# Kernel tuning notes

Measured on AMD Instinct MI355X. Metric: run time of the kernel, lower is better.

Reference implementation:

```python
import jax, jax.numpy as jnp
import numpy as np

B, C, H, W, CR = 8, 256, 128, 128, 32


def setup_inputs() -> dict:
    key = jax.random.key(0)
    ks = jax.random.split(key, 5)
    s = 0.05  # weight scale ~ conv init
    return {
        "x": jax.random.normal(ks[0], (B, C, H, W), jnp.float32),
        "Wq": jax.random.normal(ks[1], (CR, C), jnp.float32) * s,
        "bq": jnp.zeros((CR,), jnp.float32),
        "Wk": jax.random.normal(ks[2], (CR, C), jnp.float32) * s,
        "bk": jnp.zeros((CR,), jnp.float32),
        "Wv": jax.random.normal(ks[3], (CR, C), jnp.float32) * s,
        "bv": jnp.zeros((CR,), jnp.float32),
        "Wz": jax.random.normal(ks[4], (C, CR), jnp.float32) * s,
        "bz": jnp.zeros((C,), jnp.float32),
    }


def _conv1x1(w, b, x):
    # 1x1 conv == per-pixel channel matmul
    return jnp.einsum('oc,bchw->bohw', w, x) + b[None, :, None, None]


def reference(x, Wq, bq, Wk, bk, Wv, bv, Wz, bz):
    h = x.shape[2]
    q = _conv1x1(Wq, bq, x)   # (B,Cr,H,W)
    k = _conv1x1(Wk, bk, x)
    v = _conv1x1(Wv, bv, x)
    # column (height-axis) energies, -inf on diagonal to avoid double-counting self
    neg_inf_diag = jnp.where(jnp.eye(h, dtype=bool), -jnp.inf, 0.0)  # (H,H)
    energy_H = jnp.einsum('bchw,bciw->bwhi', q, k) + neg_inf_diag   # (B,W,H,H)
    energy_H = energy_H.transpose(0, 2, 1, 3)                        # (B,H,W,H)
    # row (width-axis) energies
    energy_W = jnp.einsum('bchw,bchj->bhwj', q, k)                   # (B,H,W,W)
    attn = jax.nn.softmax(jnp.concatenate([energy_H, energy_W], axis=-1), axis=-1)
    out = jnp.einsum('bciw,bhwi->bchw', v, attn[..., :h])
    out = out + jnp.einsum('bchj,bhwj->bchw', v, attn[..., h:])
    out = _conv1x1(Wz, bz, out)
    return out + x  # with_residual=True
```

## Files before the change

kernel.cpp:

```cpp
#include <hip/hip_runtime.h>
#include <stdint.h>


typedef __attribute__((ext_vector_type(8))) short bf16x8;
typedef __attribute__((ext_vector_type(4))) float f32x4;
union frag_u { uint4 u4; bf16x8 h8; };

__device__ __forceinline__ float bf2f(uint32_t u) {
  union { uint32_t i; float f; } v; v.i = u << 16; return v.f;
}
__device__ __forceinline__ float bf2f_hi(uint32_t u) {
  union { uint32_t i; float f; } v; v.i = u & 0xffff0000u; return v.f;
}
__device__ __forceinline__ uint32_t f2bf(float f) {
  union { float f; uint32_t i; } v; v.f = f;
  return (v.i + 0x7fffu + ((v.i >> 16) & 1u)) >> 16;
}
__device__ __forceinline__ void unpack8(uint4 a, float* f) {
  f[0] = bf2f(a.x); f[1] = bf2f_hi(a.x);
  f[2] = bf2f(a.y); f[3] = bf2f_hi(a.y);
  f[4] = bf2f(a.z); f[5] = bf2f_hi(a.z);
  f[6] = bf2f(a.w); f[7] = bf2f_hi(a.w);
}
__device__ __forceinline__ float ld_any(const void* p, int i, int isf32) {
  return isf32 ? ((const float*)p)[i] : bf2f(((const uint16_t*)p)[i]);
}

#define XS_SWZ(m, k)  ((m) * 40 + ((k) ^ ((((m) >> 3) & 3) << 3)))
#define P_SWZ(r, c)   ((r) * 128 + ((c) ^ (((r) & 7) << 3)))

__global__ void detect_kernel(const uint16_t* __restrict__ x, int* __restrict__ flag) {
  __shared__ int bad;
  if (threadIdx.x == 0) bad = 0;
  __syncthreads();
  int hit = 0;
#pragma unroll
  for (int s = 0; s < 16; ++s) {
    uint32_t u = x[(threadIdx.x * 16 + s) * 2];
    uint32_t e = (u >> 7) & 0xffu;
    if (e == 0u || e == 255u) hit = 1;
  }
  if (hit) atomicAdd(&bad, 1);
  __syncthreads();
  if (threadIdx.x == 0) flag[0] = (bad > 0) ? 1 : 0;
}

__global__ void prep_kernel(
    const int* __restrict__ flag,
    const void* __restrict__ Wq, const void* __restrict__ bq,
    const void* __restrict__ Wk, const void* __restrict__ bk,
    const void* __restrict__ Wv, const void* __restrict__ bv,
    const void* __restrict__ Wz, const void* __restrict__ bz,
    float* __restrict__ wb, float* __restrict__ wzf,
    float* __restrict__ bzf, uint16_t* __restrict__ wbf)
{
  int isf32 = flag[0];
  int t = blockIdx.x * 256 + threadIdx.x;
  if (t < 24576) {
    int n = t >> 8, kk = t & 255;
    int z = n >> 5, o = n & 31;
    const void* W = (z == 0) ? Wq : (z == 1) ? Wk : Wv;
    wbf[t] = (uint16_t)f2bf(ld_any(W, o * 256 + kk, isf32));
  }
  if (t < 96) {
    int z = t >> 5, o = t & 31;
    const void* bb = (z == 0) ? bq : (z == 1) ? bk : bv;
    wb[t] = ld_any(bb, o, isf32);
  }
  if (t < 8192) wzf[t] = ld_any(Wz, t, isf32);
  if (t < 256)  bzf[t] = ld_any(bz, t, isf32);
}

__global__ __launch_bounds__(256) void qkv_mfma(
    const int* __restrict__ flag, const void* __restrict__ x,
    const uint16_t* __restrict__ wbf, const float* __restrict__ wb,
    uint16_t* __restrict__ qcol, uint16_t* __restrict__ kcol,
    uint16_t* __restrict__ vcol, uint16_t* __restrict__ qrow,
    uint16_t* __restrict__ krow, uint16_t* __restrict__ vrow)
{
  __shared__ __align__(16) uint16_t Xs[128 * 40];
  int isf32 = flag[0];
  int bx = blockIdx.x;
  int b = bx >> 7, hrow = bx & 127;
  int t = threadIdx.x;
  int wv = t >> 6, L = t & 63, quad = L >> 4, l15 = L & 15;

  f32x4 acc[2][6];
#pragma unroll
  for (int mi = 0; mi < 2; ++mi)
#pragma unroll
    for (int nt = 0; nt < 6; ++nt) {
      f32x4 z0 = {0.f, 0.f, 0.f, 0.f};
      acc[mi][nt] = z0;
    }

  for (int kc = 0; kc < 8; ++kc) {
    int k0 = kc * 32;
    __syncthreads();
    if (isf32) {
      const float* xp = (const float*)x + ((size_t)b << 22)
                      + (size_t)k0 * 16384 + hrow * 128;
#pragma unroll
      for (int r = 0; r < 16; ++r) {
        int idx = r * 256 + t, k = idx >> 7, m = idx & 127;
        Xs[XS_SWZ(m, k)] = (uint16_t)f2bf(xp[(size_t)k * 16384 + m]);
      }
    } else {
      const uint16_t* xp = (const uint16_t*)x + ((size_t)b << 22)
                         + (size_t)k0 * 16384 + hrow * 128;
#pragma unroll
      for (int r = 0; r < 16; ++r) {
        int idx = r * 256 + t, k = idx >> 7, m = idx & 127;
        Xs[XS_SWZ(m, k)] = xp[(size_t)k * 16384 + m];
      }
    }
    __syncthreads();

    bf16x8 af[2];
#pragma unroll
    for (int mi = 0; mi < 2; ++mi) {
      int row = (wv * 2 + mi) * 16 + l15;
      frag_u fu;
      fu.u4 = *(const uint4*)(Xs + XS_SWZ(row, quad * 8));
      af[mi] = fu.h8;
    }
#pragma unroll
    for (int nt = 0; nt < 6; ++nt) {
      frag_u bu;
      bu.u4 = *(const uint4*)(wbf + (nt * 16 + l15) * 256 + k0 + quad * 8);
#pragma unroll
      for (int mi = 0; mi < 2; ++mi)
        acc[mi][nt] = __builtin_amdgcn_mfma_f32_16x16x32_bf16(af[mi], bu.h8, acc[mi][nt], 0, 0, 0);
    }
  }

#pragma unroll
  for (int nt = 0; nt < 6; ++nt) {
    int n = nt * 16 + l15;
    float bias = wb[n];
    int z = nt >> 1;
    int no = n & 31;
    uint16_t* colb = (z == 0) ? qcol : (z == 1) ? kcol : vcol;
    uint16_t* rowb = (z == 0) ? qrow : (z == 1) ? krow : vrow;
    size_t rowbase = (size_t)(b * 128 + hrow) * 4096;
#pragma unroll
    for (int mi = 0; mi < 2; ++mi) {
#pragma unroll
      for (int r = 0; r < 4; ++r) {
        int m = (wv * 2 + mi) * 16 + quad * 4 + r;
        uint16_t val = (uint16_t)f2bf(acc[mi][nt][r] + bias);
        rowb[rowbase + (size_t)m * 32 + no] = val;
        colb[(size_t)(b * 128 + m) * 4096 + hrow * 32 + no] = val;
      }
    }
  }
}

__global__ __launch_bounds__(256, 4) void attn_kernel(
    const uint16_t* __restrict__ q, const uint16_t* __restrict__ k,
    const uint16_t* __restrict__ v, uint16_t* __restrict__ O,
    float* __restrict__ s, int iscol)
{
  __shared__ __align__(16) uint16_t P[128 * 128];
  __shared__ __align__(16) uint16_t vT[32 * 128];

  int cid = blockIdx.x, b = cid >> 7, loc = cid & 127;
  int tid = threadIdx.x;
  const uint16_t* qc = q + (size_t)cid * 4096;
  const uint16_t* kc = k + (size_t)cid * 4096;
  const uint16_t* vc = v + (size_t)cid * 4096;

  for (int idx = tid; idx < 4096; idx += 256) {
    int ch = idx & 31, i = idx >> 5;
    vT[P_SWZ(ch, i)] = vc[idx];
  }

  int wv = tid >> 6, L = tid & 63, quad = L >> 4, l15 = L & 15;

  bf16x8 aq[2];
#pragma unroll
  for (int mi = 0; mi < 2; ++mi) {
    frag_u fu;
    fu.u4 = *(const uint4*)(qc + ((wv * 2 + mi) * 16 + l15) * 32 + quad * 8);
    aq[mi] = fu.h8;
  }
  for (int nt = 0; nt < 8; ++nt) {
    frag_u bu;
    bu.u4 = *(const uint4*)(kc + (nt * 16 + l15) * 32 + quad * 8);
    int col = nt * 16 + l15;
#pragma unroll
    for (int mi = 0; mi < 2; ++mi) {
      f32x4 z0 = {0.f, 0.f, 0.f, 0.f};
      f32x4 d = __builtin_amdgcn_mfma_f32_16x16x32_bf16(aq[mi], bu.h8, z0, 0, 0, 0);
      int row0 = (wv * 2 + mi) * 16 + quad * 4;
#pragma unroll
      for (int r = 0; r < 4; ++r) {
        float pe = __expf(d[r]);
        if (iscol && (row0 + r) == col) pe = 0.f;
        P[P_SWZ(row0 + r, col)] = (uint16_t)f2bf(pe);
      }
    }
  }
  __syncthreads();

  {
    int row = tid >> 1, hh = tid & 1;
    float ss = 0.f;
    const uint2* pr = (const uint2*)(P + row * 128 + hh * 64);
#pragma unroll 4
    for (int j = 0; j < 16; ++j) {
      uint2 u = pr[j];
      ss += bf2f(u.x); ss += bf2f_hi(u.x);
      ss += bf2f(u.y); ss += bf2f_hi(u.y);
    }
    ss += __shfl_xor(ss, 1);
    if (hh == 0) {
      size_t sbase = (size_t)b * 16384 + (iscol ? loc : loc * 128);
      s[sbase + (size_t)row * (iscol ? 128 : 1)] = ss;
    }
  }

  f32x4 acc[2][2];
#pragma unroll
  for (int mi = 0; mi < 2; ++mi)
#pragma unroll
    for (int ni = 0; ni < 2; ++ni) {
      f32x4 z0 = {0.f, 0.f, 0.f, 0.f};
      acc[mi][ni] = z0;
    }
#pragma unroll
  for (int kk = 0; kk < 4; ++kk) {
    bf16x8 ap[2], bv2[2];
#pragma unroll
    for (int mi = 0; mi < 2; ++mi) {
      int row = (wv * 2 + mi) * 16 + l15;
      frag_u fu;
      fu.u4 = *(const uint4*)(P + P_SWZ(row, kk * 32 + quad * 8));
      ap[mi] = fu.h8;
    }
#pragma unroll
    for (int ni = 0; ni < 2; ++ni) {
      int ch = ni * 16 + l15;
      frag_u fu;
      fu.u4 = *(const uint4*)(vT + P_SWZ(ch, kk * 32 + quad * 8));
      bv2[ni] = fu.h8;
    }
#pragma unroll
    for (int mi = 0; mi < 2; ++mi)
#pragma unroll
      for (int ni = 0; ni < 2; ++ni)
        acc[mi][ni] = __builtin_amdgcn_mfma_f32_16x16x32_bf16(ap[mi], bv2[ni], acc[mi][ni], 0, 0, 0);
  }

  size_t obase = (size_t)b * 524288 + (size_t)(iscol ? loc * 32 : loc * 4096);
  int orstride = iscol ? 4096 : 32;
#pragma unroll
  for (int mi = 0; mi < 2; ++mi)
#pragma unroll
    for (int ni = 0; ni < 2; ++ni) {
      int col = ni * 16 + l15;
#pragma unroll
      for (int r = 0; r < 4; ++r) {
        int row = (wv * 2 + mi) * 16 + quad * 4 + r;
        O[obase + (size_t)row * orstride + col] = (uint16_t)f2bf(acc[mi][ni][r]);
      }
    }
}

#define CSPLIT 4
__global__ __launch_bounds__(256) void combine_zres(
    const int* __restrict__ flag, const void* __restrict__ x,
    const uint16_t* __restrict__ Ocol, const uint16_t* __restrict__ Orow,
    const float* __restrict__ scol, const float* __restrict__ srow,
    const float* __restrict__ wzf, const float* __restrict__ bzf,
    void* __restrict__ out)
{
  int isf32 = flag[0];
  int bid = blockIdx.x;
  int pixblk = bid & 511;
  int cgrp = bid >> 9;
  int p = pixblk * 256 + threadIdx.x;
  int b = p >> 14;
  int rem = p & 16383;

  float inv = 1.0f / (scol[p] + srow[p]);
  float of[32];
  const uint4* c4 = (const uint4*)(Ocol + (size_t)p * 32);
  const uint4* r4 = (const uint4*)(Orow + (size_t)p * 32);
#pragma unroll
  for (int g = 0; g < 4; ++g) {
    float a[8], bb[8];
    unpack8(c4[g], a);
    unpack8(r4[g], bb);
#pragma unroll
    for (int j = 0; j < 8; ++j) of[g * 8 + j] = (a[j] + bb[j]) * inv;
  }

  int c0 = cgrp * (256 / CSPLIT);
  int c1 = c0 + (256 / CSPLIT);

  if (isf32) {
    const float* xp = (const float*)x + ((size_t)b << 22) + rem;
    float* op = (float*)out + ((size_t)b << 22) + rem;
#pragma unroll 2
    for (int c = c0; c < c1; ++c) {
      const float* wc = wzf + c * 32;
      float xv = xp[(size_t)c << 14];
      float a0 = 0.f, a1 = 0.f, a2 = 0.f, a3 = 0.f;
#pragma unroll
      for (int r = 0; r < 8; ++r) {
        a0 += wc[r]      * of[r];
        a1 += wc[8 + r]  * of[8 + r];
        a2 += wc[16 + r] * of[16 + r];
        a3 += wc[24 + r] * of[24 + r];
      }
      op[(size_t)c << 14] = bzf[c] + (a0 + a1) + (a2 + a3) + xv;
    }
  } else {
    const uint16_t* xp = (const uint16_t*)x + ((size_t)b << 22) + rem;
    uint16_t* op = (uint16_t*)out + ((size_t)b << 22) + rem;
#pragma unroll 2
    for (int c = c0; c < c1; ++c) {
      const float* wc = wzf + c * 32;
      float xv = bf2f(xp[(size_t)c << 14]);
      float a0 = 0.f, a1 = 0.f, a2 = 0.f, a3 = 0.f;
#pragma unroll
      for (int r = 0; r < 8; ++r) {
        a0 += wc[r]      * of[r];
        a1 += wc[8 + r]  * of[8 + r];
        a2 += wc[16 + r] * of[16 + r];
        a3 += wc[24 + r] * of[24 + r];
      }
      float acci = bzf[c] + (a0 + a1) + (a2 + a3) + xv;
      op[(size_t)c << 14] = (uint16_t)f2bf(acci);
    }
  }
}

extern "C" void kernel_launch(void* const* d_in, const int* in_sizes, int n_in,
                              void* d_out, int out_size, void* d_ws, size_t ws_size,
                              hipStream_t stream) {
  char* ws = (char*)d_ws;
  int*   flag = (int*)(ws);
  float* wb   = (float*)(ws + 256);
  float* wzf  = (float*)(ws + 1024);
  float* bzf  = (float*)(ws + 33792);
  uint16_t* wbf = (uint16_t*)(ws + 34816);
  uint16_t* qt = (uint16_t*)(ws + 147456);
  uint16_t* kt = qt + 4194304;
  uint16_t* vt = kt + 4194304;
  uint16_t* qr = vt + 4194304;
  uint16_t* kr = qr + 4194304;
  uint16_t* vr = kr + 4194304;
  uint16_t* Ocol = (uint16_t*)(ws + 50479104);
  uint16_t* Orow = (uint16_t*)(ws + 58867712);
  float* scol = (float*)(ws + 67256320);
  float* srow = (float*)(ws + 67780608);

  detect_kernel<<<1, 256, 0, stream>>>((const uint16_t*)d_in[0], flag);
  prep_kernel<<<96, 256, 0, stream>>>(flag, d_in[1], d_in[2], d_in[3], d_in[4],
                                      d_in[5], d_in[6], d_in[7], d_in[8],
                                      wb, wzf, bzf, wbf);
  qkv_mfma<<<1024, 256, 0, stream>>>(flag, d_in[0], wbf, wb,
                                     qt, kt, vt, qr, kr, vr);
  attn_kernel<<<1024, 256, 0, stream>>>(qt, kt, vt, Ocol, scol, 1);
  attn_kernel<<<1024, 256, 0, stream>>>(qr, kr, vr, Orow, srow, 0);
  combine_zres<<<512 * CSPLIT, 256, 0, stream>>>(flag, d_in[0], Ocol, Orow,
                                                 scol, srow, wzf, bzf, d_out);
}
```

Before: 345.1 us.

## Prefetch x tiles into registers, merge attention launches, tweak unroll and bounds

The QKV projection kernel now loads the next 32-channel chunk of x into registers while MFMAs run on the current chunk held in shared memory. This software-pipelines global loads against compute. The column and row attention passes are merged into a single 2048-block launch, with the block index choosing which pass it runs, which removes one launch and the tail between them. Separately, qkv_mfma gets a min-blocks launch bound and the combine loop unroll goes from 2 to 4. Both raise register pressure, and the 16-register prefetch buffer could cap occupancy.

Result: no change. 340.0 us (-1.5%).

```diff
diff --git a/kernel.cpp b/kernel.cpp
--- a/kernel.cpp
+++ b/kernel.cpp
@@ -71,7 +71,7 @@
   if (t < 256)  bzf[t] = ld_any(bz, t, isf32);
 }
 
-__global__ __launch_bounds__(256) void qkv_mfma(
+__global__ __launch_bounds__(256, 4) void qkv_mfma(
     const int* __restrict__ flag, const void* __restrict__ x,
     const uint16_t* __restrict__ wbf, const float* __restrict__ wb,
     uint16_t* __restrict__ qcol, uint16_t* __restrict__ kcol,
@@ -84,6 +84,10 @@
   int b = bx >> 7, hrow = bx & 127;
   int t = threadIdx.x;
   int wv = t >> 6, L = t & 63, quad = L >> 4, l15 = L & 15;
+  int m_t = t & 127, kh = t >> 7;
+
+  const float*    xf = (const float*)x    + ((size_t)b << 22) + hrow * 128 + m_t;
+  const uint16_t* xh = (const uint16_t*)x + ((size_t)b << 22) + hrow * 128 + m_t;
 
   f32x4 acc[2][6];
 #pragma unroll
@@ -94,28 +98,37 @@
       acc[mi][nt] = z0;
     }
 
+  uint32_t xs[16];
+  auto issue = [&](int kcn) {
+    if (isf32) {
+#pragma unroll
+      for (int r = 0; r < 16; ++r)
+        xs[r] = __float_as_uint(xf[(size_t)(kcn * 32 + 2 * r + kh) * 16384]);
+    } else {
+#pragma unroll
+      for (int r = 0; r < 16; ++r)
+        xs[r] = xh[(size_t)(kcn * 32 + 2 * r + kh) * 16384];
+    }
+  };
+
+  issue(0);
+
   for (int kc = 0; kc < 8; ++kc) {
-    int k0 = kc * 32;
     __syncthreads();
     if (isf32) {
-      const float* xp = (const float*)x + ((size_t)b << 22)
-                      + (size_t)k0 * 16384 + hrow * 128;
-#pragma unroll
-      for (int r = 0; r < 16; ++r) {
-        int idx = r * 256 + t, k = idx >> 7, m = idx & 127;
-        Xs[XS_SWZ(m, k)] = (uint16_t)f2bf(xp[(size_t)k * 16384 + m]);
-      }
+#pragma unroll
+      for (int r = 0; r < 16; ++r)
+        Xs[XS_SWZ(m_t, 2 * r + kh)] = (uint16_t)f2bf(__uint_as_float(xs[r]));
     } else {
-      const uint16_t* xp = (const uint16_t*)x + ((size_t)b << 22)
-                         + (size_t)k0 * 16384 + hrow * 128;
-#pragma unroll
-      for (int r = 0; r < 16; ++r) {
-        int idx = r * 256 + t, k = idx >> 7, m = idx & 127;
-        Xs[XS_SWZ(m, k)] = xp[(size_t)k * 16384 + m];
-      }
+#pragma unroll
+      for (int r = 0; r < 16; ++r)
+        Xs[XS_SWZ(m_t, 2 * r + kh)] = (uint16_t)xs[r];
     }
     __syncthreads();
 
+    if (kc < 7) issue(kc + 1);
+
+    int k0 = kc * 32;
     bf16x8 af[2];
 #pragma unroll
     for (int mi = 0; mi < 2; ++mi) {
@@ -157,18 +170,24 @@
 }
 
 __global__ __launch_bounds__(256, 4) void attn_kernel(
-    const uint16_t* __restrict__ q, const uint16_t* __restrict__ k,
-    const uint16_t* __restrict__ v, uint16_t* __restrict__ O,
-    float* __restrict__ s, int iscol)
+    const uint16_t* __restrict__ qc_, const uint16_t* __restrict__ kc_,
+    const uint16_t* __restrict__ vc_, const uint16_t* __restrict__ qr_,
+    const uint16_t* __restrict__ kr_, const uint16_t* __restrict__ vr_,
+    uint16_t* __restrict__ Ocol, uint16_t* __restrict__ Orow,
+    float* __restrict__ scol, float* __restrict__ srow)
 {
   __shared__ __align__(16) uint16_t P[128 * 128];
   __shared__ __align__(16) uint16_t vT[32 * 128];
 
-  int cid = blockIdx.x, b = cid >> 7, loc = cid & 127;
+  int bidx = blockIdx.x;
+  int iscol = (bidx < 1024) ? 1 : 0;
+  int cid = bidx & 1023, b = cid >> 7, loc = cid & 127;
   int tid = threadIdx.x;
-  const uint16_t* qc = q + (size_t)cid * 4096;
-  const uint16_t* kc = k + (size_t)cid * 4096;
-  const uint16_t* vc = v + (size_t)cid * 4096;
+  const uint16_t* qc = (iscol ? qc_ : qr_) + (size_t)cid * 4096;
+  const uint16_t* kc = (iscol ? kc_ : kr_) + (size_t)cid * 4096;
+  const uint16_t* vc = (iscol ? vc_ : vr_) + (size_t)cid * 4096;
+  uint16_t* O = iscol ? Ocol : Orow;
+  float*    s = iscol ? scol : srow;
 
   for (int idx = tid; idx < 4096; idx += 256) {
     int ch = idx & 31, i = idx >> 5;
@@ -302,7 +321,7 @@
   if (isf32) {
     const float* xp = (const float*)x + ((size_t)b << 22) + rem;
     float* op = (float*)out + ((size_t)b << 22) + rem;
-#pragma unroll 2
+#pragma unroll 4
     for (int c = c0; c < c1; ++c) {
       const float* wc = wzf + c * 32;
       float xv = xp[(size_t)c << 14];
@@ -319,7 +338,7 @@
   } else {
     const uint16_t* xp = (const uint16_t*)x + ((size_t)b << 22) + rem;
     uint16_t* op = (uint16_t*)out + ((size_t)b << 22) + rem;
-#pragma unroll 2
+#pragma unroll 4
     for (int c = c0; c < c1; ++c) {
       const float* wc = wzf + c * 32;
       float xv = bf2f(xp[(size_t)c << 14]);
@@ -363,8 +382,8 @@
                                       wb, wzf, bzf, wbf);
   qkv_mfma<<<1024, 256, 0, stream>>>(flag, d_in[0], wbf, wb,
                                      qt, kt, vt, qr, kr, vr);
-  attn_kernel<<<1024, 256, 0, stream>>>(qt, kt, vt, Ocol, scol, 1);
-  attn_kernel<<<1024, 256, 0, stream>>>(qr, kr, vr, Orow, srow, 0);
+  attn_kernel<<<2048, 256, 0, stream>>>(qt, kt, vt, qr, kr, vr,
+                                        Ocol, Orow, scol, srow);
   combine_zres<<<512 * CSPLIT, 256, 0, stream>>>(flag, d_in[0], Ocol, Orow,
                                                  scol, srow, wzf, bzf, d_out);
 }
```
